# Kernel optimization log

Hardware: AMD Instinct MI355X
Metric: run time of the kernel (lower is better)

## Reference

```python
import jax, jax.numpy as jnp
import numpy as np

WIN = 256  # window_size from init_kwargs


def _stream_attn(q, k, v, win, hollow):
    """Banded sliding-window attention.

    hollow=False (s-stream): key j attended iff 0 <= i - j < win (last `win` tokens incl. self).
    hollow=True  (c-stream): key j attended iff win <= i - j < 2*win (tokens [i-2W+1, i-W]).
    Returns (out [B,S,H,D], lse [B,H,S]) with lse = -inf for fully-masked rows.
    """
    B, S, H, D = q.shape
    nb = S // win
    scale = D ** -0.5
    qb = q.reshape(B, nb, win, H, D)
    kb = k.reshape(B, nb, win, H, D)
    vb = v.reshape(B, nb, win, H, D)
    pad = ((0, 0), (2, 0), (0, 0), (0, 0), (0, 0))
    kp = jnp.pad(kb, pad)
    vp = jnp.pad(vb, pad)
    k_ctx = jnp.concatenate([kp[:, t:t + nb] for t in range(3)], axis=2)  # [B,nb,3W,H,D]
    v_ctx = jnp.concatenate([vp[:, t:t + nb] for t in range(3)], axis=2)
    lq = jnp.arange(win)[:, None]
    kk = jnp.arange(3 * win)[None, :]
    t_blk = kk // win
    lk = kk % win
    rel = (2 - t_blk) * win + lq - lk  # i - j, shape [W, 3W]
    if hollow:
        wmask = (rel >= win) & (rel < 2 * win)
    else:
        wmask = (rel >= 0) & (rel < win)
    blk_ok = (jnp.arange(nb)[:, None] - 2 + (jnp.arange(3 * win) // win)[None, :]) >= 0  # [nb,3W]
    mask = wmask[None] & blk_ok[:, None, :]  # [nb, W, 3W]
    logits = jnp.einsum('bnqhd,bnkhd->bnhqk', qb, k_ctx) * scale  # [B,nb,H,W,3W]
    logits = jnp.where(mask[None, :, None], logits, -jnp.inf)
    m = jnp.max(logits, axis=-1)  # [B,nb,H,W]
    ms = jnp.where(jnp.isneginf(m), 0.0, m)
    p = jnp.exp(logits - ms[..., None])
    denom = jnp.sum(p, axis=-1)  # [B,nb,H,W]
    out = jnp.einsum('bnhqk,bnkhd->bnqhd', p, v_ctx)  # [B,nb,W,H,D]
    safe = jnp.where(denom > 0, denom, 1.0)
    out = out / jnp.moveaxis(safe, 2, 3)[..., None]
    lse = jnp.where(denom > 0, jnp.log(safe) + m, -jnp.inf)  # [B,nb,H,W]
    out = out.reshape(B, S, H, D)
    lse = jnp.moveaxis(lse, 1, 2).reshape(B, H, S)
    return out, lse


def _merge(out_c, lse_c, out_s, lse_s):
    # faithful jax version of merge_attn_states_torch (LSE online-softmax merge)
    m = jnp.maximum(lse_c, lse_s)
    ms = jnp.where(jnp.isneginf(m), 0.0, m)
    ec = jnp.exp(lse_c - ms)
    es = jnp.exp(lse_s - ms)
    se = ec + es  # s-stream always has >=1 key (self), so se > 0
    c_scale = jnp.moveaxis(ec / se, 1, 2)[..., None]  # [B,S,H,1]
    s_scale = jnp.moveaxis(es / se, 1, 2)[..., None]
    return out_c * c_scale + out_s * s_scale


def setup_inputs() -> dict:
    key = jax.random.key(0)
    k1, k2, k3 = jax.random.split(key, 3)
    B, S, H, D = 2, 2048, 16, 128
    return {
        'query': jax.random.normal(k1, (B, S, H, D), dtype=jnp.float32),
        'key': jax.random.normal(k2, (B, S, H, D), dtype=jnp.float32),
        'value': jax.random.normal(k3, (B, S, H, D), dtype=jnp.float32),
    }


def reference(query, key, value):
    out_c, lse_c = _stream_attn(query, key, value, WIN, hollow=True)   # c-stream: [i-2W, i-W]
    out_s, lse_s = _stream_attn(query, key, value, WIN, hollow=False)  # s-stream: last W tokens
    return _merge(out_c, lse_c, out_s, lse_s)
```

## Files before the change

kernel.cpp:

```cpp
#include <hip/hip_runtime.h>
#include <math.h>

#define S_LEN 2048
#define NH    16
#define DD    128
#define SROW  (NH*DD)
#define WIN2  512
#define BQ    128
#define BK    64
#define RSQ   136
#define RS    72

typedef __bf16 bf16x8 __attribute__((ext_vector_type(8)));
typedef __bf16 bf16x4 __attribute__((ext_vector_type(4)));
typedef float  f32x4  __attribute__((ext_vector_type(4)));

__device__ __forceinline__ f32x4 mfma16(bf16x8 a, bf16x8 b, f32x4 c) {
    return __builtin_amdgcn_mfma_f32_16x16x32_bf16(a, b, c, 0, 0, 0);
}

__device__ __forceinline__ unsigned int pack_bf16(float lo, float hi) {
    return (unsigned int)__builtin_bit_cast(unsigned short, (__bf16)lo)
         | ((unsigned int)__builtin_bit_cast(unsigned short, (__bf16)hi) << 16);
}

#define OFF_VT 8704
#define OFF_P  17920
#define SMEM_ELEMS 27136

__global__ __launch_bounds__(512, 4)
void swattn_kernel(const float* __restrict__ Qg, const float* __restrict__ Kg,
                   const float* __restrict__ Vg, float* __restrict__ Og) {
    __shared__ __align__(16) __bf16 smem[SMEM_ELEMS];

    const int t   = threadIdx.x;
    const int w   = t >> 6;
    const int l   = t & 63;
    const int r16 = l & 15;
    const int g4  = l >> 4;
    const int Qlo = blockIdx.x * BQ;
    const int h   = blockIdx.y;
    const int b   = blockIdx.z;

    const size_t bh = ((size_t)b * S_LEN) * SROW + (size_t)h * DD;
    const float C1 = 0.08838834764831845f * 1.44269504088896340f;

    for (int it = 0; it < 8; ++it) {
        int f   = it * 512 + t;
        int q_l = f >> 5;
        int dq  = (f & 31) * 4;
        const float4 v = *(const float4*)&Qg[bh + (size_t)(Qlo + q_l) * SROW + dq];
        bf16x4 o4 = { (__bf16)(v.x * C1), (__bf16)(v.y * C1),
                      (__bf16)(v.z * C1), (__bf16)(v.w * C1) };
        *(bf16x4*)&smem[q_l * RSQ + dq] = o4;
    }
    __syncthreads();

    bf16x8 qf[4];
#pragma unroll
    for (int sl = 0; sl < 4; ++sl)
        qf[sl] = *(const bf16x8*)&smem[(w*16 + r16) * RSQ + sl*32 + g4*8];
    __syncthreads();

    const f32x4 zero4 = {0.f, 0.f, 0.f, 0.f};
    f32x4 oacc[8];
#pragma unroll
    for (int dg = 0; dg < 8; ++dg) oacc[dg] = zero4;
    float m_run = -1e4f;
    float l_run = 0.f;

    const int q_w = Qlo + w * 16;
    const int gv = l >> 5;
    const int rv = l & 31;

    int cb = Qlo - (WIN2 - 1);
    if (cb < 0) cb = 0;
    cb &= ~(BK - 1);
    const int Qhi = Qlo + BQ - 1;

    for (int c0 = cb; c0 <= Qhi; c0 += BK) {
        for (int it = 0; it < 4; ++it) {
            int f   = it * 512 + t;
            int k_l = f >> 5;
            int dq  = (f & 31) * 4;
            const float4 v = *(const float4*)&Kg[bh + (size_t)(c0 + k_l) * SROW + dq];
            bf16x4 o4 = { (__bf16)v.x, (__bf16)v.y, (__bf16)v.z, (__bf16)v.w };
            *(bf16x4*)&smem[k_l * RSQ + dq] = o4;
        }
        for (int it = 0; it < 4; ++it) {
            int k0l = w * 8 + it * 2;
            const float4 v4 = *(const float4*)&Vg[bh + (size_t)(c0 + k0l + gv) * SROW + 4*rv];
            float ox = __shfl_xor(v4.x, 32);
            float oy = __shfl_xor(v4.y, 32);
            float oz = __shfl_xor(v4.z, 32);
            float ow = __shfl_xor(v4.w, 32);
            float lo0, hi0, lo1, hi1; int d0;
            if (gv == 0) { lo0 = v4.x; hi0 = ox;   lo1 = v4.y; hi1 = oy;   d0 = 4*rv; }
            else         { lo0 = oz;   hi0 = v4.z; lo1 = ow;   hi1 = v4.w; d0 = 4*rv + 2; }
            int col = k0l ^ ((rv & 7) << 3);
            *(unsigned int*)&smem[OFF_VT + (d0    ) * RS + col] = pack_bf16(lo0, hi0);
            *(unsigned int*)&smem[OFF_VT + (d0 + 1) * RS + col] = pack_bf16(lo1, hi1);
        }
        __syncthreads();

        const bool act = (q_w + 15 >= c0) && (q_w <= c0 + (BK - 1) + (WIN2 - 1));
        if (act) {
            f32x4 st[4] = { zero4, zero4, zero4, zero4 };
#pragma unroll
            for (int sl = 0; sl < 4; ++sl)
#pragma unroll
                for (int kg = 0; kg < 4; ++kg) {
                    bf16x8 kf = *(const bf16x8*)&smem[(kg*16 + r16) * RSQ + sl*32 + g4*8];
                    st[kg] = mfma16(kf, qf[sl], st[kg]);
                }

            const bool fv = (q_w >= c0 + (BK - 1)) && (q_w + 15 <= c0 + (WIN2 - 1));
            if (!fv) {
                int iq = q_w + r16;
#pragma unroll
                for (int kg = 0; kg < 4; ++kg) {
                    int relb = iq - (c0 + kg*16 + 4*g4);
#pragma unroll
                    for (int rg = 0; rg < 4; ++rg) {
                        bool ok = ((unsigned)(relb - rg)) < (unsigned)WIN2;
                        st[kg][rg] = ok ? st[kg][rg] : -1e30f;
                    }
                }
            }

            float mc = -1e30f;
#pragma unroll
            for (int kg = 0; kg < 4; ++kg)
#pragma unroll
                for (int rg = 0; rg < 4; ++rg) mc = fmaxf(mc, st[kg][rg]);
            mc = fmaxf(mc, __shfl_xor(mc, 16));
            mc = fmaxf(mc, __shfl_xor(mc, 32));
            float mn = fmaxf(m_run, mc);
            float alpha = exp2f(m_run - mn);
            m_run = mn;
            float sum = 0.f;
#pragma unroll
            for (int kg = 0; kg < 4; ++kg)
#pragma unroll
                for (int rg = 0; rg < 4; ++rg) {
                    float p = exp2f(st[kg][rg] - mn);
                    st[kg][rg] = p;
                    sum += p;
                }
            sum += __shfl_xor(sum, 16);
            sum += __shfl_xor(sum, 32);
            l_run = l_run * alpha + sum;

#pragma unroll
            for (int kg = 0; kg < 4; ++kg) {
                f32x4 pv = st[kg];
                bf16x4 p4 = { (__bf16)pv[0], (__bf16)pv[1], (__bf16)pv[2], (__bf16)pv[3] };
                *(bf16x4*)&smem[OFF_P + (w*16 + r16) * RS + kg*16 + 4*g4] = p4;
            }

#pragma unroll
            for (int dg = 0; dg < 8; ++dg)
#pragma unroll
                for (int rg = 0; rg < 4; ++rg) oacc[dg][rg] *= alpha;

#pragma unroll
            for (int ks = 0; ks < 2; ++ks) {
                bf16x8 pf = *(const bf16x8*)&smem[OFF_P + (w*16 + r16) * RS + ks*32 + g4*8];
#pragma unroll
                for (int dg = 0; dg < 8; ++dg) {
                    int col = (ks*32 + g4*8) ^ (32*(dg&1) + 8*(r16>>2));
                    bf16x8 vf = *(const bf16x8*)&smem[OFF_VT + (dg*16 + r16) * RS + col];
                    oacc[dg] = mfma16(vf, pf, oacc[dg]);
                }
            }
        }
        __syncthreads();
    }

    float inv = 1.f / l_run;
    int q = q_w + r16;
    size_t base = bh + (size_t)q * SROW;
#pragma unroll
    for (int dg = 0; dg < 8; ++dg) {
        f32x4 o = oacc[dg];
        float4 res = { o[0]*inv, o[1]*inv, o[2]*inv, o[3]*inv };
        *(float4*)&Og[base + dg*16 + 4*g4] = res;
    }
}

extern "C" void kernel_launch(void* const* d_in, const int* in_sizes, int n_in,
                              void* d_out, int out_size, void* d_ws, size_t ws_size,
                              hipStream_t stream) {
    const float* q = (const float*)d_in[0];
    const float* k = (const float*)d_in[1];
    const float* v = (const float*)d_in[2];
    float* o = (float*)d_out;
    int B = in_sizes[0] / (S_LEN * NH * DD);
    dim3 grid(S_LEN / BQ, NH, B);
    swattn_kernel<<<grid, 512, 0, stream>>>(q, k, v, o);
}
```

Measured before the change: 174.6 us.

## Prefetch next K/V tile into registers during compute and raise MFMA priority

Global loads of the next K and V tile are issued into registers before the current tile's QK and PV matmuls. They are converted and written to shared memory only after a barrier, so global memory latency overlaps with compute instead of stalling each iteration. The MFMA sections are also wrapped in s_setprio so waves doing matrix math get issue priority. The cost is 32 more live registers per thread at a launch bound of 512 threads x 4, which risks spills or lower occupancy, plus an extra barrier per iteration.

```diff
diff --git a/kernel.cpp b/kernel.cpp
--- a/kernel.cpp
+++ b/kernel.cpp
@@ -73,23 +73,29 @@
     const int gv = l >> 5;
     const int rv = l & 31;
 
+    const int kRow = t >> 5;
+    const int kCol = (t & 31) * 4;
+    const float* Kp = Kg + bh + kCol;
+    const float* Vp = Vg + bh + (size_t)(w*8 + gv) * SROW + 4*rv;
+
     int cb = Qlo - (WIN2 - 1);
     if (cb < 0) cb = 0;
     cb &= ~(BK - 1);
     const int Qhi = Qlo + BQ - 1;
 
-    for (int c0 = cb; c0 <= Qhi; c0 += BK) {
+    float4 kv[4], vv[4];
+
+    auto stage_write = [&]() {
+#pragma unroll
         for (int it = 0; it < 4; ++it) {
-            int f   = it * 512 + t;
-            int k_l = f >> 5;
-            int dq  = (f & 31) * 4;
-            const float4 v = *(const float4*)&Kg[bh + (size_t)(c0 + k_l) * SROW + dq];
+            const float4 v = kv[it];
             bf16x4 o4 = { (__bf16)v.x, (__bf16)v.y, (__bf16)v.z, (__bf16)v.w };
-            *(bf16x4*)&smem[k_l * RSQ + dq] = o4;
-        }
+            *(bf16x4*)&smem[(kRow + it*16) * RSQ + kCol] = o4;
+        }
+#pragma unroll
         for (int it = 0; it < 4; ++it) {
-            int k0l = w * 8 + it * 2;
-            const float4 v4 = *(const float4*)&Vg[bh + (size_t)(c0 + k0l + gv) * SROW + 4*rv];
+            const int k0l = w*8 + it*2;
+            const float4 v4 = vv[it];
             float ox = __shfl_xor(v4.x, 32);
             float oy = __shfl_xor(v4.y, 32);
             float oz = __shfl_xor(v4.z, 32);
@@ -101,11 +107,33 @@
             *(unsigned int*)&smem[OFF_VT + (d0    ) * RS + col] = pack_bf16(lo0, hi0);
             *(unsigned int*)&smem[OFF_VT + (d0 + 1) * RS + col] = pack_bf16(lo1, hi1);
         }
-        __syncthreads();
+    };
+
+#pragma unroll
+    for (int it = 0; it < 4; ++it)
+        kv[it] = *(const float4*)(Kp + (size_t)(cb + kRow + it*16) * SROW);
+#pragma unroll
+    for (int it = 0; it < 4; ++it)
+        vv[it] = *(const float4*)(Vp + (size_t)(cb + it*2) * SROW);
+    stage_write();
+    __syncthreads();
+
+    for (int c0 = cb; c0 <= Qhi; c0 += BK) {
+        const int cn  = c0 + BK;
+        const bool pfn = (cn <= Qhi);
+        if (pfn) {
+#pragma unroll
+            for (int it = 0; it < 4; ++it)
+                kv[it] = *(const float4*)(Kp + (size_t)(cn + kRow + it*16) * SROW);
+#pragma unroll
+            for (int it = 0; it < 4; ++it)
+                vv[it] = *(const float4*)(Vp + (size_t)(cn + it*2) * SROW);
+        }
 
         const bool act = (q_w + 15 >= c0) && (q_w <= c0 + (BK - 1) + (WIN2 - 1));
         if (act) {
             f32x4 st[4] = { zero4, zero4, zero4, zero4 };
+            __builtin_amdgcn_s_setprio(1);
 #pragma unroll
             for (int sl = 0; sl < 4; ++sl)
 #pragma unroll
@@ -113,6 +141,7 @@
                     bf16x8 kf = *(const bf16x8*)&smem[(kg*16 + r16) * RSQ + sl*32 + g4*8];
                     st[kg] = mfma16(kf, qf[sl], st[kg]);
                 }
+            __builtin_amdgcn_s_setprio(0);
 
             const bool fv = (q_w >= c0 + (BK - 1)) && (q_w + 15 <= c0 + (WIN2 - 1));
             if (!fv) {
@@ -163,6 +192,7 @@
 #pragma unroll
                 for (int rg = 0; rg < 4; ++rg) oacc[dg][rg] *= alpha;
 
+            __builtin_amdgcn_s_setprio(1);
 #pragma unroll
             for (int ks = 0; ks < 2; ++ks) {
                 bf16x8 pf = *(const bf16x8*)&smem[OFF_P + (w*16 + r16) * RS + ks*32 + g4*8];
@@ -173,7 +203,10 @@
                     oacc[dg] = mfma16(vf, pf, oacc[dg]);
                 }
             }
-        }
+            __builtin_amdgcn_s_setprio(0);
+        }
+        __syncthreads();
+        if (pfn) stage_write();
         __syncthreads();
     }
 
```

After: 200.3 us. +14.8%, slower.

## Prefetch next K/V chunk into registers during compute and raise MFMA priority

Applied to the files above, without the earlier changes.

The K/V tile loads move out of the critical path. The next chunk's global loads are issued into registers before the current chunk is computed, then converted and written to LDS after a barrier. The MFMA sections are also wrapped in s_setprio to favour the compute waves. This is meant to hide global load latency behind the matrix work, at the cost of extra registers (eight float4 per thread) and an extra barrier per iteration, which may reduce occupancy under the launch bounds.

```diff
diff --git a/kernel.cpp b/kernel.cpp
--- a/kernel.cpp
+++ b/kernel.cpp
@@ -27,6 +27,37 @@
 #define OFF_VT 8704
 #define OFF_P  17920
 #define SMEM_ELEMS 27136
+
+#define CVT_K(v, it) do {                                                     \
+    bf16x4 o4_ = { (__bf16)(v).x, (__bf16)(v).y, (__bf16)(v).z, (__bf16)(v).w }; \
+    *(bf16x4*)&smem[(kRow + (it)*16) * RSQ + kCol] = o4_; } while (0)
+
+#define CVT_V(v4, it) do {                                                    \
+    const int k0l_ = w*8 + (it)*2;                                            \
+    float ox_ = __shfl_xor((v4).x, 32);                                       \
+    float oy_ = __shfl_xor((v4).y, 32);                                       \
+    float oz_ = __shfl_xor((v4).z, 32);                                       \
+    float ow_ = __shfl_xor((v4).w, 32);                                       \
+    float lo0_, hi0_, lo1_, hi1_; int d0_;                                    \
+    if (gv == 0) { lo0_ = (v4).x; hi0_ = ox_;    lo1_ = (v4).y; hi1_ = oy_;    d0_ = 4*rv; } \
+    else         { lo0_ = oz_;    hi0_ = (v4).z; lo1_ = ow_;    hi1_ = (v4).w; d0_ = 4*rv + 2; } \
+    int col_ = k0l_ ^ ((rv & 7) << 3);     \
+    *(unsigned int*)&smem[OFF_VT + (d0_    ) * RS + col_] = pack_bf16(lo0_, hi0_); \
+    *(unsigned int*)&smem[OFF_VT + (d0_ + 1) * RS + col_] = pack_bf16(lo1_, hi1_); } while (0)
+
+#define STAGE_WRITE() do {                                                    \
+    CVT_K(kv0, 0); CVT_K(kv1, 1); CVT_K(kv2, 2); CVT_K(kv3, 3);               \
+    CVT_V(vv0, 0); CVT_V(vv1, 1); CVT_V(vv2, 2); CVT_V(vv3, 3); } while (0)
+
+#define LOAD_CHUNK(c) do {                                                    \
+    kv0 = *(const float4*)(Kp + (size_t)((c) + kRow +  0) * SROW);            \
+    kv1 = *(const float4*)(Kp + (size_t)((c) + kRow + 16) * SROW);            \
+    kv2 = *(const float4*)(Kp + (size_t)((c) + kRow + 32) * SROW);            \
+    kv3 = *(const float4*)(Kp + (size_t)((c) + kRow + 48) * SROW);            \
+    vv0 = *(const float4*)(Vp + (size_t)((c) + 0) * SROW);                    \
+    vv1 = *(const float4*)(Vp + (size_t)((c) + 2) * SROW);                    \
+    vv2 = *(const float4*)(Vp + (size_t)((c) + 4) * SROW);                    \
+    vv3 = *(const float4*)(Vp + (size_t)((c) + 6) * SROW); } while (0)
 
 __global__ __launch_bounds__(512, 4)
 void swattn_kernel(const float* __restrict__ Qg, const float* __restrict__ Kg,
@@ -73,39 +104,31 @@
     const int gv = l >> 5;
     const int rv = l & 31;
 
+    const int kRow = t >> 5;
+    const int kCol = (t & 31) * 4;
+    const float* Kp = Kg + bh + kCol;
+    const float* Vp = Vg + bh + (size_t)(w*8 + gv) * SROW + 4*rv;
+
     int cb = Qlo - (WIN2 - 1);
     if (cb < 0) cb = 0;
     cb &= ~(BK - 1);
     const int Qhi = Qlo + BQ - 1;
 
+    float4 kv0, kv1, kv2, kv3, vv0, vv1, vv2, vv3;
+
+    LOAD_CHUNK(cb);
+    STAGE_WRITE();
+    __syncthreads();
+
     for (int c0 = cb; c0 <= Qhi; c0 += BK) {
-        for (int it = 0; it < 4; ++it) {
-            int f   = it * 512 + t;
-            int k_l = f >> 5;
-            int dq  = (f & 31) * 4;
-            const float4 v = *(const float4*)&Kg[bh + (size_t)(c0 + k_l) * SROW + dq];
-            bf16x4 o4 = { (__bf16)v.x, (__bf16)v.y, (__bf16)v.z, (__bf16)v.w };
-            *(bf16x4*)&smem[k_l * RSQ + dq] = o4;
-        }
-        for (int it = 0; it < 4; ++it) {
-            int k0l = w * 8 + it * 2;
-            const float4 v4 = *(const float4*)&Vg[bh + (size_t)(c0 + k0l + gv) * SROW + 4*rv];
-            float ox = __shfl_xor(v4.x, 32);
-            float oy = __shfl_xor(v4.y, 32);
-            float oz = __shfl_xor(v4.z, 32);
-            float ow = __shfl_xor(v4.w, 32);
-            float lo0, hi0, lo1, hi1; int d0;
-            if (gv == 0) { lo0 = v4.x; hi0 = ox;   lo1 = v4.y; hi1 = oy;   d0 = 4*rv; }
-            else         { lo0 = oz;   hi0 = v4.z; lo1 = ow;   hi1 = v4.w; d0 = 4*rv + 2; }
-            int col = k0l ^ ((rv & 7) << 3);
-            *(unsigned int*)&smem[OFF_VT + (d0    ) * RS + col] = pack_bf16(lo0, hi0);
-            *(unsigned int*)&smem[OFF_VT + (d0 + 1) * RS + col] = pack_bf16(lo1, hi1);
-        }
-        __syncthreads();
+        const int cn  = c0 + BK;
+        const bool pfn = (cn <= Qhi);
+        if (pfn) LOAD_CHUNK(cn);
 
         const bool act = (q_w + 15 >= c0) && (q_w <= c0 + (BK - 1) + (WIN2 - 1));
         if (act) {
             f32x4 st[4] = { zero4, zero4, zero4, zero4 };
+            __builtin_amdgcn_s_setprio(1);
 #pragma unroll
             for (int sl = 0; sl < 4; ++sl)
 #pragma unroll
@@ -113,6 +136,7 @@
                     bf16x8 kf = *(const bf16x8*)&smem[(kg*16 + r16) * RSQ + sl*32 + g4*8];
                     st[kg] = mfma16(kf, qf[sl], st[kg]);
                 }
+            __builtin_amdgcn_s_setprio(0);
 
             const bool fv = (q_w >= c0 + (BK - 1)) && (q_w + 15 <= c0 + (WIN2 - 1));
             if (!fv) {
@@ -163,6 +187,7 @@
 #pragma unroll
                 for (int rg = 0; rg < 4; ++rg) oacc[dg][rg] *= alpha;
 
+            __builtin_amdgcn_s_setprio(1);
 #pragma unroll
             for (int ks = 0; ks < 2; ++ks) {
                 bf16x8 pf = *(const bf16x8*)&smem[OFF_P + (w*16 + r16) * RS + ks*32 + g4*8];
@@ -173,7 +198,10 @@
                     oacc[dg] = mfma16(vf, pf, oacc[dg]);
                 }
             }
+            __builtin_amdgcn_s_setprio(0);
         }
+        __syncthreads();
+        if (pfn) STAGE_WRITE();
         __syncthreads();
     }
 
```

Measured after the change: 203.4 us. +16.5%, slower.
